# Optimization experiments

Hardware: AMD Instinct MI355X
Metric: run time of the kernel (lower is better)

The kernel has to match this reference:

```python
import jax, jax.numpy as jnp
import numpy as np

B, NT, NC, NN = 2, 64, 1024, 1024
C, H = 1024, 16
HD = C // H
N = NT + NC + NN
EPS = 1e-5
NEG = -1e30


def _ln(t, w, b):
    # LayerNorm over last dim (head_dim), torch eps=1e-5
    mu = jnp.mean(t, axis=-1, keepdims=True)
    var = jnp.mean(jnp.square(t - mu), axis=-1, keepdims=True)
    return (t - mu) * jax.lax.rsqrt(var + EPS) * w + b


def _rope(q, k, pos):
    # q,k: [B,H,S,HD]; pos: [B,S]; rotate-half RoPE, base 10000
    hd = q.shape[-1]
    half = hd // 2
    inv_freq = 1.0 / (10000.0 ** (jnp.arange(half, dtype=jnp.float32) / half))
    ang = pos.astype(jnp.float32)[:, None, :, None] * inv_freq  # [B,1,S,half]
    cos, sin = jnp.cos(ang), jnp.sin(ang)
    def rot(t):
        t1, t2 = t[..., :half], t[..., half:]
        return jnp.concatenate([t1 * cos - t2 * sin, t2 * cos + t1 * sin], axis=-1)
    return rot(q), rot(k)


def setup_inputs() -> dict:
    key = jax.random.key(0)
    ks = jax.random.split(key, 4)
    s = 0.02
    return {
        "x": jax.random.normal(ks[0], (B, N, C), jnp.float32),
        "position_ids": jnp.broadcast_to(jnp.arange(NC + NN, dtype=jnp.int32), (B, NC + NN)),
        "text_position_ids": jnp.broadcast_to(jnp.arange(NT, dtype=jnp.int32), (B, NT)),
        "attention_mask": jnp.tril(jnp.ones((N, N), dtype=bool)),
        "n_text": NT, "n_clean": NC, "n_noised": NN,
        "qkv_w": jax.random.normal(ks[1], (3, 3 * C, C), jnp.float32) * s,
        "qkv_b": jnp.zeros((3, 3 * C), jnp.float32),
        "qn_w": jnp.ones((3, HD), jnp.float32),
        "qn_b": jnp.zeros((3, HD), jnp.float32),
        "kn_w": jnp.ones((3, HD), jnp.float32),
        "kn_b": jnp.zeros((3, HD), jnp.float32),
        "proj_w": jax.random.normal(ks[2], (3, C, C), jnp.float32) * s,
        "proj_b": jnp.zeros((3, C), jnp.float32),
    }


def reference(x, position_ids, text_position_ids, attention_mask, n_text, n_clean, n_noised,
              qkv_w, qkv_b, qn_w, qn_b, kn_w, kn_b, proj_w, proj_b):
    Bx, Nx, Cx = x.shape
    hd = qn_w.shape[-1]
    nh = Cx // hd
    b0, b1 = n_text, n_text + n_clean
    segs = (x[:, :b0], x[:, b0:b1], x[:, b1:])  # text / clean / noised

    qs, kks, vvs = [], [], []
    for i, xs in enumerate(segs):
        S = xs.shape[1]
        qkv = jnp.einsum('bsc,oc->bso', xs, qkv_w[i]) + qkv_b[i]
        qkv = qkv.reshape(Bx, S, 3, nh, hd).transpose(2, 0, 3, 1, 4)  # [3,B,H,S,hd]
        q = _ln(qkv[0], qn_w[i], qn_b[i])
        k = _ln(qkv[1], kn_w[i], kn_b[i])
        qs.append(q); kks.append(k); vvs.append(qkv[2])

    img_q = jnp.concatenate([qs[1], qs[2]], axis=2)
    img_k = jnp.concatenate([kks[1], kks[2]], axis=2)
    img_q, img_k = _rope(img_q, img_k, position_ids)
    txt_q, txt_k = _rope(qs[0], kks[0], text_position_ids)

    q = jnp.concatenate([txt_q, img_q], axis=2)
    k = jnp.concatenate([txt_k, img_k], axis=2)
    v = jnp.concatenate(vvs, axis=2)

    scale = 1.0 / np.sqrt(hd).astype(np.float32)
    scores = jnp.einsum('bhqd,bhkd->bhqk', q, k) * scale
    scores = jnp.where(attention_mask, scores, NEG)
    attn = jax.nn.softmax(scores, axis=-1)
    out = jnp.einsum('bhqk,bhkd->bhqd', attn, v)
    out = out.transpose(0, 2, 1, 3).reshape(Bx, Nx, Cx)

    o_segs = (out[:, :b0], out[:, b0:b1], out[:, b1:])
    outs = [jnp.einsum('bsc,oc->bso', o_segs[i], proj_w[i]) + proj_b[i] for i in range(3)]
    return jnp.concatenate(outs, axis=1)
```

## Files before the change

### kernel.cpp

```cpp
#include <hip/hip_runtime.h>
#include <hip/hip_bf16.h>

#define BB   2
#define NT   64
#define NC   1024
#define NN   1024
#define NTOK (NT + NC + NN)
#define CC   1024
#define HH   16
#define HD   64
#define K3   (3 * CC)
#define EPSV 1e-5f

typedef __attribute__((ext_vector_type(8))) short short8;
typedef __attribute__((ext_vector_type(4))) float f32x4;
typedef __attribute__((ext_vector_type(4))) float float4v;

__device__ __forceinline__ short bf16raw(float x) {
    __hip_bfloat16 h = __float2bfloat16(x);
    return *(short*)&h;
}

#define GL_LDS(gptr, lptr) \
    __builtin_amdgcn_global_load_lds( \
        (const __attribute__((address_space(1))) void*)(gptr), \
        (__attribute__((address_space(3))) void*)(lptr), 16, 0, 0)

__constant__ signed char QB_tab[33] =
    {16,16,16,15,15,15,14,14,14,13,13,13,12,12,12,11,11,10,10,9,9,8,8,7,7,6,6,5,4,3,2,1,0};
__constant__ signed char CH_tab[33] =
    { 0, 1, 2, 0, 1, 2, 0, 1, 2, 0, 1, 2, 0, 1, 2, 0, 1, 0, 1,0,1,0,1,0,1,0,1,0,0,0,0,0,0};

__global__ __launch_bounds__(256) void cast_all(
    const float* __restrict__ s0, const float* __restrict__ s1, const float* __restrict__ s2,
    __hip_bfloat16* __restrict__ d0, __hip_bfloat16* __restrict__ d1, __hip_bfloat16* __restrict__ d2,
    int n0, int n1, int n2)
{
    int i = blockIdx.x * 256 + threadIdx.x;
    int stride = gridDim.x * 256;
    int ntot = n0 + n1 + n2;
    for (; i < ntot; i += stride) {
        const float* sp; short* dp; int j;
        if (i < n0)            { sp = s0; dp = (short*)d0; j = i; }
        else if (i < n0 + n1)  { sp = s1; dp = (short*)d1; j = i - n0; }
        else                   { sp = s2; dp = (short*)d2; j = i - n0 - n1; }
        float4v v = *(const float4v*)(sp + (size_t)j * 4);
        short4 o;
        o.x = bf16raw(v.x); o.y = bf16raw(v.y); o.z = bf16raw(v.z); o.w = bf16raw(v.w);
        *(short4*)(dp + (size_t)j * 4) = o;
    }
}

__global__ __launch_bounds__(256) void gemm_qkv(
    const __hip_bfloat16* __restrict__ A,
    const __hip_bfloat16* __restrict__ Wb,
    const float* __restrict__ biasb,
    const float* __restrict__ qn_w, const float* __restrict__ qn_b,
    const float* __restrict__ kn_w, const float* __restrict__ kn_b,
    __hip_bfloat16* __restrict__ Q,
    __hip_bfloat16* __restrict__ Kg,
    __hip_bfloat16* __restrict__ Vt)
{
    __shared__ short lds[32768];
    short* buf = lds;

    int tid = threadIdx.x;
    int lane = tid & 63, w = tid >> 6;
    int l15 = lane & 15, quad = lane >> 4;
    int wm = w >> 1, wn = w & 1;
    int r7 = l15 & 7;

    int y = blockIdx.y;
    int seg, tm;
    if (y < 16)      { seg = 1; tm = y * 128; }
    else if (y < 32) { seg = 2; tm = (y - 16) * 128; }
    else             { seg = 0; tm = 0; }
    int S = (seg == 0) ? 64 : 1024;
    int seg_start = (seg == 0) ? 0 : (seg == 1 ? NT : NT + NC);
    const short* W = (const short*)Wb + (size_t)seg * K3 * CC;
    const float* bias = biasb + (size_t)seg * K3;
    int tileN = blockIdx.x * 128;

    const short* aptr[4];
    const short* bptr[4];
#pragma unroll
    for (int j = 0; j < 4; ++j) {
        int c = j * 256 + tid;
        int row = c >> 3, u = (c & 7) ^ (row & 7);
        int ar = tm + row;
        int arow = (ar / S) * NTOK + seg_start + (ar % S);
        aptr[j] = (const short*)A + (size_t)arow * CC + u * 8;
        bptr[j] = W + (size_t)(tileN + row) * CC + u * 8;
    }

    f32x4 zero = {0.f, 0.f, 0.f, 0.f};
    f32x4 acc[4][4];
#pragma unroll
    for (int mb = 0; mb < 4; ++mb)
#pragma unroll
        for (int nb = 0; nb < 4; ++nb) acc[mb][nb] = zero;

#pragma unroll
    for (int j = 0; j < 4; ++j) {
        int c8 = (j * 256 + tid) * 8;
        GL_LDS(aptr[j], lds + c8);
        GL_LDS(bptr[j], lds + 8192 + c8);
    }
    __syncthreads();

    int cur = 0;
    for (int k0 = 64; k0 <= CC; k0 += 64) {
        short* As = lds + cur * 16384;
        short* Bs = As + 8192;
        if (k0 < CC) {
            short* An = lds + (cur ^ 1) * 16384;
#pragma unroll
            for (int j = 0; j < 4; ++j) {
                int c8 = (j * 256 + tid) * 8;
                GL_LDS(aptr[j] + k0, An + c8);
                GL_LDS(bptr[j] + k0, An + 8192 + c8);
            }
        }

#pragma unroll
        for (int s = 0; s < 2; ++s) {
            int sx = ((s * 4 + quad) ^ r7) * 8;
            short8 af[4], bf[4];
#pragma unroll
            for (int mb = 0; mb < 4; ++mb)
                af[mb] = *(const short8*)&As[(wm * 64 + mb * 16 + l15) * 64 + sx];
#pragma unroll
            for (int nb = 0; nb < 4; ++nb)
                bf[nb] = *(const short8*)&Bs[(wn * 64 + nb * 16 + l15) * 64 + sx];
#pragma unroll
            for (int mb = 0; mb < 4; ++mb)
#pragma unroll
                for (int nb = 0; nb < 4; ++nb)
                    acc[mb][nb] = __builtin_amdgcn_mfma_f32_16x16x32_bf16(af[mb], bf[nb], acc[mb][nb], 0, 0, 0);
        }
        __syncthreads();
        cur ^= 1;
    }

    int sect = tileN >> 10;

    if (sect < 2) {
        const float* nw = (sect == 0 ? qn_w : kn_w) + seg * HD;
        const float* nbv = (sect == 0 ? qn_b : kn_b) + seg * HD;
        float lw[4], lb[4], bcol[4];
#pragma unroll
        for (int nb = 0; nb < 4; ++nb) {
            lw[nb] = nw[nb * 16 + l15];
            lb[nb] = nbv[nb * 16 + l15];
            bcol[nb] = bias[tileN + wn * 64 + nb * 16 + l15];
        }
        float qscale = (sect == 0) ? 0.125f : 1.0f;

        float invf0 = expf(-9.210340371976184f * (float)l15 * (1.0f / 32.0f));
        float invf1 = expf(-9.210340371976184f * (float)(16 + l15) * (1.0f / 32.0f));
        float cd0, sd0, cd1, sd1;
        sincosf(invf0, &sd0, &cd0);
        sincosf(invf1, &sd1, &cd1);

#pragma unroll
        for (int mb = 0; mb < 4; ++mb) {
            int tok0 = wm * 64 + mb * 16 + quad * 4;
            int ar0 = tm + tok0;
            int nloc0 = ar0 % S;
            int pos0 = (seg == 0) ? nloc0 : (seg_start + nloc0 - NT);
            float c0, s0, c1, s1v;
            sincosf((float)pos0 * invf0, &s0, &c0);
            sincosf((float)pos0 * invf1, &s1v, &c1);

#pragma unroll
            for (int r = 0; r < 4; ++r) {
                int tok = tok0 + r;
                float v[4];
#pragma unroll
                for (int nb = 0; nb < 4; ++nb) v[nb] = acc[mb][nb][r] + bcol[nb];

                float t1 = v[0] + v[1] + v[2] + v[3];
                float t2 = v[0] * v[0] + v[1] * v[1] + v[2] * v[2] + v[3] * v[3];
#pragma unroll
                for (int off = 8; off >= 1; off >>= 1) {
                    t1 += __shfl_xor(t1, off);
                    t2 += __shfl_xor(t2, off);
                }
                float mu = t1 * (1.0f / 64.0f);
                float var = t2 * (1.0f / 64.0f) - mu * mu;
                float rstd = rsqrtf(var + EPSV);
#pragma unroll
                for (int nb = 0; nb < 4; ++nb) v[nb] = (v[nb] - mu) * rstd * lw[nb] + lb[nb];

                short* bp = &buf[tok * 134 + wn * 64];
                bp[0 * 16 + l15] = bf16raw((v[0] * c0 - v[2] * s0) * qscale);
                bp[1 * 16 + l15] = bf16raw((v[1] * c1 - v[3] * s1v) * qscale);
                bp[2 * 16 + l15] = bf16raw((v[2] * c0 + v[0] * s0) * qscale);
                bp[3 * 16 + l15] = bf16raw((v[3] * c1 + v[1] * s1v) * qscale);

                float nc0 = c0 * cd0 - s0 * sd0, ns0 = s0 * cd0 + c0 * sd0;
                float nc1 = c1 * cd1 - s1v * sd1, ns1 = s1v * cd1 + c1 * sd1;
                c0 = nc0; s0 = ns0; c1 = nc1; s1v = ns1;
            }
        }
        __syncthreads();
        __hip_bfloat16* dst = (sect == 0) ? Q : Kg;
        int head_base = (tileN & 1023) >> 6;
#pragma unroll
        for (int it = 0; it < 8; ++it) {
            int idx = it * 256 + tid;
            int tok = idx >> 4, cc = (idx & 15) * 8;
            int ar = tm + tok;
            int bb = ar / S;
            int nloc = seg_start + (ar % S);
            int hh2 = head_base + (cc >> 6), d = cc & 63;
            *(short8*)((short*)dst + ((size_t)(bb * HH + hh2) * NTOK + nloc) * HD + d) =
                *(const short8*)&buf[tok * 134 + cc];
        }
    } else {
        float bcol[4];
#pragma unroll
        for (int nb = 0; nb < 4; ++nb) bcol[nb] = bias[tileN + wn * 64 + nb * 16 + l15];
#pragma unroll
        for (int mb = 0; mb < 4; ++mb) {
#pragma unroll
            for (int r = 0; r < 4; ++r) {
                int tok = wm * 64 + mb * 16 + quad * 4 + r;
#pragma unroll
                for (int nb = 0; nb < 4; ++nb) {
                    int col = wn * 64 + nb * 16 + l15;
                    buf[col * 134 + tok] = bf16raw(acc[mb][nb][r] + bcol[nb]);
                }
            }
        }
        __syncthreads();
#pragma unroll
        for (int it = 0; it < 8; ++it) {
            int idx = it * 256 + tid;
            int row = idx >> 4;
            int tc = (idx & 15) * 8;
            int vcol = (tileN - 2048) + row;
            int h = vcol >> 6, d = vcol & 63;
            int ar = tm + tc;
            int bb = ar / S;
            int nloc = seg_start + (ar % S);
            short8 val = *(const short8*)&buf[row * 134 + tc];
            *(short8*)((short*)Vt + ((size_t)(bb * HH + h) * HD + d) * NTOK + nloc) = val;
        }
    }
}

__global__ __launch_bounds__(256) void gemm_proj(
    const __hip_bfloat16* __restrict__ A,
    const __hip_bfloat16* __restrict__ Wb,
    const float* __restrict__ biasb,
    float* __restrict__ Cout)
{
    __shared__ short lds[24576];

    int tid = threadIdx.x;
    int lane = tid & 63, w = tid >> 6;
    int l15 = lane & 15, quad = lane >> 4;
    int wm = w >> 1, wn = w & 1;
    int r7 = l15 & 7;

    int y = blockIdx.y;
    int seg, tm;
    if (y < 32)      { seg = 1; tm = y * 64; }
    else if (y < 64) { seg = 2; tm = (y - 32) * 64; }
    else             { seg = 0; tm = (y - 64) * 64; }
    int S = (seg == 0) ? 64 : 1024;
    int seg_start = (seg == 0) ? 0 : (seg == 1 ? NT : NT + NC);
    const short* W = (const short*)Wb + (size_t)seg * CC * CC;
    const float* bias = biasb + (size_t)seg * CC;
    int tileN = blockIdx.x * 128;

    const short* aptr[2];
    const short* bptr[4];
#pragma unroll
    for (int j = 0; j < 2; ++j) {
        int c = j * 256 + tid;
        int row = c >> 3, u = (c & 7) ^ (row & 7);
        int ar = tm + row;
        int arow = (ar / S) * NTOK + seg_start + (ar % S);
        aptr[j] = (const short*)A + (size_t)arow * CC + u * 8;
    }
#pragma unroll
    for (int j = 0; j < 4; ++j) {
        int c = j * 256 + tid;
        int row = c >> 3, u = (c & 7) ^ (row & 7);
        bptr[j] = W + (size_t)(tileN + row) * CC + u * 8;
    }

    f32x4 zero = {0.f, 0.f, 0.f, 0.f};
    f32x4 acc[2][4];
#pragma unroll
    for (int mb = 0; mb < 2; ++mb)
#pragma unroll
        for (int nb = 0; nb < 4; ++nb) acc[mb][nb] = zero;

#pragma unroll
    for (int j = 0; j < 2; ++j)
        GL_LDS(aptr[j], lds + (j * 256 + tid) * 8);
#pragma unroll
    for (int j = 0; j < 4; ++j)
        GL_LDS(bptr[j], lds + 4096 + (j * 256 + tid) * 8);
    __syncthreads();

    int cur = 0;
    for (int k0 = 64; k0 <= CC; k0 += 64) {
        short* As = lds + cur * 12288;
        short* Bs = As + 4096;
        if (k0 < CC) {
            short* An = lds + (cur ^ 1) * 12288;
#pragma unroll
            for (int j = 0; j < 2; ++j)
                GL_LDS(aptr[j] + k0, An + (j * 256 + tid) * 8);
#pragma unroll
            for (int j = 0; j < 4; ++j)
                GL_LDS(bptr[j] + k0, An + 4096 + (j * 256 + tid) * 8);
        }

#pragma unroll
        for (int s = 0; s < 2; ++s) {
            int sx = ((s * 4 + quad) ^ r7) * 8;
            short8 af[2], bf[4];
#pragma unroll
            for (int mb = 0; mb < 2; ++mb)
                af[mb] = *(const short8*)&As[(wm * 32 + mb * 16 + l15) * 64 + sx];
#pragma unroll
            for (int nb = 0; nb < 4; ++nb)
                bf[nb] = *(const short8*)&Bs[(wn * 64 + nb * 16 + l15) * 64 + sx];
#pragma unroll
            for (int mb = 0; mb < 2; ++mb)
#pragma unroll
                for (int nb = 0; nb < 4; ++nb)
                    acc[mb][nb] = __builtin_amdgcn_mfma_f32_16x16x32_bf16(af[mb], bf[nb], acc[mb][nb], 0, 0, 0);
        }
        __syncthreads();
        cur ^= 1;
    }

#pragma unroll
    for (int mb = 0; mb < 2; ++mb) {
#pragma unroll
        for (int r = 0; r < 4; ++r) {
            int ar = tm + wm * 32 + mb * 16 + quad * 4 + r;
            int crow = (ar / S) * NTOK + seg_start + (ar % S);
            float* cp = Cout + (size_t)crow * CC + tileN;
#pragma unroll
            for (int nb = 0; nb < 4; ++nb) {
                int col = wn * 64 + nb * 16 + l15;
                cp[col] = acc[mb][nb][r] + bias[tileN + col];
            }
        }
    }
}

__global__ __launch_bounds__(512) void attn_part(
    const __hip_bfloat16* __restrict__ Q,
    const __hip_bfloat16* __restrict__ Kg,
    const __hip_bfloat16* __restrict__ Vt,
    __hip_bfloat16* __restrict__ O,
    float* __restrict__ Opart,
    float* __restrict__ lpart)
{
    __shared__ short Ks[2][4096];
    __shared__ short Vs[2][4096];
    __shared__ short Ps[8][16 * 72];

    int tid = threadIdx.x;
    int lane = tid & 63, w = tid >> 6;
    int quad = lane >> 4, l15 = lane & 15;
    int r7 = l15 & 7;
    int bh = blockIdx.y, b = bh >> 4, h = bh & 15;

    int e = blockIdx.x;
    int qb = QB_tab[e], c = CH_tab[e];
    int q0 = qb * 128;
    int nt = 2 * qb + 2; if (nt > 33) nt = 33;
    int t0 = c * 12, t1 = t0 + 12; if (t1 > nt) t1 = nt;
    bool direct = (nt <= 12);

    size_t base = (size_t)bh * NTOK * HD;

    int qrow = q0 + w * 16 + l15;
    int qr_c = qrow < NTOK ? qrow : NTOK - 1;
    short8 qf0 = *(const short8*)((const short*)Q + base + (size_t)qr_c * HD + quad * 8);
    short8 qf1 = *(const short8*)((const short*)Q + base + (size_t)qr_c * HD + 32 + quad * 8);

    int srow = tid >> 3;
    int su = (tid & 7) ^ (srow & 7);
    const short* kptr = (const short*)Kg + base + (size_t)srow * HD + su * 8;
    const short* vptr = (const short*)Vt + base + (size_t)srow * NTOK + su * 8;
    int c8 = tid * 8;

    f32x4 zero = {0.f, 0.f, 0.f, 0.f};
    f32x4 oacc[4] = {zero, zero, zero, zero};
    float l[4] = {0.f, 0.f, 0.f, 0.f};

    int qmax_w = q0 + w * 16 + 15;
    int sx0 = (quad ^ r7) * 8;
    int sx1 = ((4 + quad) ^ r7) * 8;

    GL_LDS(kptr + (size_t)(t0 * 64) * HD, Ks[0] + c8);
    GL_LDS(vptr + t0 * 64, Vs[0] + c8);
    __syncthreads();

    int cur = 0;
    for (int t = t0; t < t1; ++t) {
        if (t + 1 < t1) {
            GL_LDS(kptr + (size_t)((t + 1) * 64) * HD, Ks[cur ^ 1] + c8);
            GL_LDS(vptr + (t + 1) * 64, Vs[cur ^ 1] + c8);
        }

        if (t * 64 <= qmax_w) {
            f32x4 s[4];
#pragma unroll
            for (int kb = 0; kb < 4; ++kb) {
                int krow = (kb * 16 + l15) * 64;
                short8 kf0 = *(const short8*)&Ks[cur][krow + sx0];
                short8 kf1 = *(const short8*)&Ks[cur][krow + sx1];
                f32x4 z = zero;
                z = __builtin_amdgcn_mfma_f32_16x16x32_bf16(qf0, kf0, z, 0, 0, 0);
                z = __builtin_amdgcn_mfma_f32_16x16x32_bf16(qf1, kf1, z, 0, 0, 0);
                s[kb] = z;
            }

#pragma unroll
            for (int r = 0; r < 4; ++r) {
                int qg = q0 + w * 16 + quad * 4 + r;
#pragma unroll
                for (int kb = 0; kb < 4; ++kb) {
                    int kgk = t * 64 + kb * 16 + l15;
                    float p = (kgk <= qg) ? __expf(s[kb][r]) : 0.f;
                    Ps[w][(quad * 4 + r) * 72 + kb * 16 + l15] = bf16raw(p);
                    l[r] += p;
                }
            }

            __builtin_amdgcn_wave_barrier();

#pragma unroll
            for (int sl = 0; sl < 2; ++sl) {
                short8 pf = *(const short8*)&Ps[w][l15 * 72 + sl * 32 + quad * 8];
                int vsx = ((sl * 4 + quad) ^ r7) * 8;
#pragma unroll
                for (int db = 0; db < 4; ++db) {
                    short8 vf = *(const short8*)&Vs[cur][(db * 16 + l15) * 64 + vsx];
                    oacc[db] = __builtin_amdgcn_mfma_f32_16x16x32_bf16(pf, vf, oacc[db], 0, 0, 0);
                }
            }
        }

        __syncthreads();
        cur ^= 1;
    }

#pragma unroll
    for (int r = 0; r < 4; ++r) {
#pragma unroll
        for (int off = 8; off >= 1; off >>= 1) l[r] += __shfl_xor(l[r], off);
    }

    if (direct) {
#pragma unroll
        for (int r = 0; r < 4; ++r) {
            int qg = q0 + w * 16 + quad * 4 + r;
            float inv_l = 1.0f / l[r];
#pragma unroll
            for (int db = 0; db < 4; ++db) {
                O[(size_t)(b * NTOK + qg) * CC + h * HD + db * 16 + l15] =
                    __float2bfloat16(oacc[db][r] * inv_l);
            }
        }
    } else {
        int pidx = (bh * 17 + qb) * 3 + c;
        float* op = Opart + (size_t)pidx * (128 * 64);
#pragma unroll
        for (int r = 0; r < 4; ++r) {
            int q = w * 16 + quad * 4 + r;
#pragma unroll
            for (int db = 0; db < 4; ++db)
                op[q * 64 + db * 16 + l15] = oacc[db][r];
            if (l15 == 0) lpart[pidx * 128 + q] = l[r];
        }
    }
}

__global__ __launch_bounds__(512) void attn_comb(
    const float* __restrict__ Opart, const float* __restrict__ lpart,
    __hip_bfloat16* __restrict__ O)
{
    __shared__ float ls[128];
    int tid = threadIdx.x;
    int qb = 6 + blockIdx.x;
    int bh = blockIdx.y, b = bh >> 4, h = bh & 15;
    int nt = 2 * qb + 2; if (nt > 33) nt = 33;
    int nch = (nt + 11) / 12;
    int q0 = qb * 128;
    int pbase = (bh * 17 + qb) * 3;

    if (tid < 128) {
        float s = 0.f;
        for (int cc = 0; cc < nch; ++cc) s += lpart[(pbase + cc) * 128 + tid];
        ls[tid] = 1.0f / s;
    }
    __syncthreads();

#pragma unroll
    for (int k = 0; k < 16; ++k) {
        int elem = k * 512 + tid;
        int q = elem >> 6, d = elem & 63;
        int qg = q0 + q;
        if (qg >= NTOK) continue;
        float s = 0.f;
        for (int cc = 0; cc < nch; ++cc)
            s += Opart[(size_t)(pbase + cc) * (128 * 64) + elem];
        O[(size_t)(b * NTOK + qg) * CC + h * HD + d] = __float2bfloat16(s * ls[q]);
    }
}

extern "C" void kernel_launch(void* const* d_in, const int* in_sizes, int n_in,
                              void* d_out, int out_size, void* d_ws, size_t ws_size,
                              hipStream_t stream) {
    const float* x      = (const float*)d_in[0];
    const float* qkv_w  = (const float*)d_in[7];
    const float* qkv_b  = (const float*)d_in[8];
    const float* qn_w   = (const float*)d_in[9];
    const float* qn_b   = (const float*)d_in[10];
    const float* kn_w   = (const float*)d_in[11];
    const float* kn_b   = (const float*)d_in[12];
    const float* proj_w = (const float*)d_in[13];
    const float* proj_b = (const float*)d_in[14];
    float* out = (float*)d_out;

    const size_t n_x    = (size_t)BB * NTOK * CC;
    const size_t n_qkvw = (size_t)3 * K3 * CC;
    const size_t n_prjw = (size_t)3 * CC * CC;
    const size_t n_part = (size_t)32 * 17 * 3;

    __hip_bfloat16* x_bf    = (__hip_bfloat16*)d_ws;
    __hip_bfloat16* qkvw_bf = x_bf + n_x;
    __hip_bfloat16* prjw_bf = qkvw_bf + n_qkvw;
    __hip_bfloat16* Qbf  = prjw_bf + n_prjw;
    __hip_bfloat16* Kbf  = Qbf + n_x;
    __hip_bfloat16* Vtbf = Kbf + n_x;
    float* Opart = (float*)(Vtbf + n_x);
    float* lpart = Opart + n_part * (128 * 64);
    __hip_bfloat16* attn_bf = x_bf;

    cast_all<<<1024, 256, 0, stream>>>(x, qkv_w, proj_w, x_bf, qkvw_bf, prjw_bf,
                                       (int)(n_x / 4), (int)(n_qkvw / 4), (int)(n_prjw / 4));

    gemm_qkv<<<dim3(K3 / 128, 33), 256, 0, stream>>>(
        x_bf, qkvw_bf, qkv_b,
        qn_w, qn_b, kn_w, kn_b, Qbf, Kbf, Vtbf);

    attn_part<<<dim3(33, BB * HH), 512, 0, stream>>>(Qbf, Kbf, Vtbf, attn_bf, Opart, lpart);

    attn_comb<<<dim3(11, BB * HH), 512, 0, stream>>>(Opart, lpart, attn_bf);

    gemm_proj<<<dim3(CC / 128, 66), 256, 0, stream>>>(attn_bf, prjw_bf, proj_b, out);
}
```

Measured before the change: 264.8 us.

## Load V directly to registers, double K tiles per barrier, use exp2 with prescaled Q

The attention kernel stops staging V in LDS and reads V fragments straight from global memory into registers, overlapping those loads with the QK MFMAs. K staging now uses four LDS buffers, handling two key tiles per __syncthreads. The Q scale folds in log2(e) so softmax can use the hardware exp2, and fully unmasked tiles skip the per-element causal compare. It also adds s_setprio around MFMA blocks and an occupancy hint in launch_bounds, at the cost of uncoalesced, higher-latency V reads from global memory.

Result: slower. 308.5 us (+16.5%).

```diff
diff --git a/kernel.cpp b/kernel.cpp
--- a/kernel.cpp
+++ b/kernel.cpp
@@ -154,7 +154,7 @@
             lb[nb] = nbv[nb * 16 + l15];
             bcol[nb] = bias[tileN + wn * 64 + nb * 16 + l15];
         }
-        float qscale = (sect == 0) ? 0.125f : 1.0f;
+        float qscale = (sect == 0) ? 0.18033688011112042f : 1.0f;
 
         float invf0 = expf(-9.210340371976184f * (float)l15 * (1.0f / 32.0f));
         float invf1 = expf(-9.210340371976184f * (float)(16 + l15) * (1.0f / 32.0f));
@@ -357,7 +357,7 @@
     }
 }
 
-__global__ __launch_bounds__(512) void attn_part(
+__global__ __launch_bounds__(512, 4) void attn_part(
     const __hip_bfloat16* __restrict__ Q,
     const __hip_bfloat16* __restrict__ Kg,
     const __hip_bfloat16* __restrict__ Vt,
@@ -365,8 +365,7 @@
     float* __restrict__ Opart,
     float* __restrict__ lpart)
 {
-    __shared__ short Ks[2][4096];
-    __shared__ short Vs[2][4096];
+    __shared__ short Ks[4][4096];
     __shared__ short Ps[8][16 * 72];
 
     int tid = threadIdx.x;
@@ -392,70 +391,102 @@
     int srow = tid >> 3;
     int su = (tid & 7) ^ (srow & 7);
     const short* kptr = (const short*)Kg + base + (size_t)srow * HD + su * 8;
-    const short* vptr = (const short*)Vt + base + (size_t)srow * NTOK + su * 8;
+    const short* vrow = (const short*)Vt + base;
     int c8 = tid * 8;
 
     f32x4 zero = {0.f, 0.f, 0.f, 0.f};
     f32x4 oacc[4] = {zero, zero, zero, zero};
     float l[4] = {0.f, 0.f, 0.f, 0.f};
 
-    int qmax_w = q0 + w * 16 + 15;
+    int qmin_w = q0 + w * 16;
+    int qmax_w = qmin_w + 15;
     int sx0 = (quad ^ r7) * 8;
     int sx1 = ((4 + quad) ^ r7) * 8;
 
-    GL_LDS(kptr + (size_t)(t0 * 64) * HD, Ks[0] + c8);
-    GL_LDS(vptr + t0 * 64, Vs[0] + c8);
-    __syncthreads();
-
-    int cur = 0;
-    for (int t = t0; t < t1; ++t) {
-        if (t + 1 < t1) {
-            GL_LDS(kptr + (size_t)((t + 1) * 64) * HD, Ks[cur ^ 1] + c8);
-            GL_LDS(vptr + (t + 1) * 64, Vs[cur ^ 1] + c8);
-        }
-
-        if (t * 64 <= qmax_w) {
-            f32x4 s[4];
-#pragma unroll
-            for (int kb = 0; kb < 4; ++kb) {
-                int krow = (kb * 16 + l15) * 64;
-                short8 kf0 = *(const short8*)&Ks[cur][krow + sx0];
-                short8 kf1 = *(const short8*)&Ks[cur][krow + sx1];
-                f32x4 z = zero;
-                z = __builtin_amdgcn_mfma_f32_16x16x32_bf16(qf0, kf0, z, 0, 0, 0);
-                z = __builtin_amdgcn_mfma_f32_16x16x32_bf16(qf1, kf1, z, 0, 0, 0);
-                s[kb] = z;
-            }
-
+#define STAGE_K(t, bi) GL_LDS(kptr + (size_t)((t) * 64) * HD, Ks[bi] + c8)
+
+    auto tile = [&](int t, int buf) {
+        if (t * 64 > qmax_w) return;
+        const short* Kb = Ks[buf];
+
+        short8 vf0[4], vf1[4];
+#pragma unroll
+        for (int db = 0; db < 4; ++db)
+            vf0[db] = *(const short8*)(vrow + (size_t)(db * 16 + l15) * NTOK + t * 64 + quad * 8);
+
+        f32x4 s[4];
+        __builtin_amdgcn_s_setprio(1);
+#pragma unroll
+        for (int kb = 0; kb < 4; ++kb) {
+            int krow = (kb * 16 + l15) * 64;
+            short8 kf0 = *(const short8*)&Kb[krow + sx0];
+            short8 kf1 = *(const short8*)&Kb[krow + sx1];
+            f32x4 z = zero;
+            z = __builtin_amdgcn_mfma_f32_16x16x32_bf16(qf0, kf0, z, 0, 0, 0);
+            z = __builtin_amdgcn_mfma_f32_16x16x32_bf16(qf1, kf1, z, 0, 0, 0);
+            s[kb] = z;
+        }
+        __builtin_amdgcn_s_setprio(0);
+
+#pragma unroll
+        for (int db = 0; db < 4; ++db)
+            vf1[db] = *(const short8*)(vrow + (size_t)(db * 16 + l15) * NTOK + t * 64 + 32 + quad * 8);
+
+        if (t * 64 + 63 <= qmin_w) {
+#pragma unroll
+            for (int r = 0; r < 4; ++r)
+#pragma unroll
+                for (int kb = 0; kb < 4; ++kb) {
+                    float p = __builtin_amdgcn_exp2f(s[kb][r]);
+                    Ps[w][(quad * 4 + r) * 72 + kb * 16 + l15] = bf16raw(p);
+                    l[r] += p;
+                }
+        } else {
 #pragma unroll
             for (int r = 0; r < 4; ++r) {
                 int qg = q0 + w * 16 + quad * 4 + r;
 #pragma unroll
                 for (int kb = 0; kb < 4; ++kb) {
                     int kgk = t * 64 + kb * 16 + l15;
-                    float p = (kgk <= qg) ? __expf(s[kb][r]) : 0.f;
+                    float p = (kgk <= qg) ? __builtin_amdgcn_exp2f(s[kb][r]) : 0.f;
                     Ps[w][(quad * 4 + r) * 72 + kb * 16 + l15] = bf16raw(p);
                     l[r] += p;
                 }
             }
-
-            __builtin_amdgcn_wave_barrier();
-
-#pragma unroll
-            for (int sl = 0; sl < 2; ++sl) {
-                short8 pf = *(const short8*)&Ps[w][l15 * 72 + sl * 32 + quad * 8];
-                int vsx = ((sl * 4 + quad) ^ r7) * 8;
-#pragma unroll
-                for (int db = 0; db < 4; ++db) {
-                    short8 vf = *(const short8*)&Vs[cur][(db * 16 + l15) * 64 + vsx];
-                    oacc[db] = __builtin_amdgcn_mfma_f32_16x16x32_bf16(pf, vf, oacc[db], 0, 0, 0);
-                }
-            }
-        }
+        }
+
+        __builtin_amdgcn_wave_barrier();
+
+        __builtin_amdgcn_s_setprio(1);
+#pragma unroll
+        for (int sl = 0; sl < 2; ++sl) {
+            short8 pf = *(const short8*)&Ps[w][l15 * 72 + sl * 32 + quad * 8];
+#pragma unroll
+            for (int db = 0; db < 4; ++db)
+                oacc[db] = __builtin_amdgcn_mfma_f32_16x16x32_bf16(
+                    pf, sl ? vf1[db] : vf0[db], oacc[db], 0, 0, 0);
+        }
+        __builtin_amdgcn_s_setprio(0);
+        __builtin_amdgcn_wave_barrier();
+    };
+
+    int nload = t1 - t0;
+    STAGE_K(t0, 0);
+    if (nload > 1) STAGE_K(t0 + 1, 1);
+    __syncthreads();
+
+    int bi = 0;
+    for (int t = t0; t < t1; t += 2) {
+        if (t + 2 < t1) STAGE_K(t + 2, bi ^ 2);
+        if (t + 3 < t1) STAGE_K(t + 3, bi ^ 3);
+
+        tile(t, bi);
+        if (t + 1 < t1) tile(t + 1, bi ^ 1);
 
         __syncthreads();
-        cur ^= 1;
-    }
+        bi ^= 2;
+    }
+#undef STAGE_K
 
 #pragma unroll
     for (int r = 0; r < 4; ++r) {
```
